# Kernel tuning notes

Measured on AMD Instinct MI355X. Metric: run time of the kernel, lower is better.

Reference implementation:

```python
import jax, jax.numpy as jnp
import numpy as np

B, C, N, K, G = 4, 128, 4096, 9, 4


def setup_inputs() -> dict:
    key = jax.random.key(0)
    ks = jax.random.split(key, 4)
    s = 0.05
    return {
        "features": jax.random.normal(ks[0], (B, C, N, 1), jnp.float32),
        # Attn.linear: Conv2d(2C -> C, 1x1)
        "w_lin": jax.random.normal(ks[1], (C, 2 * C), jnp.float32) * s,
        "b_lin": jnp.zeros((C,), jnp.float32),
        # atten_weight_conv: Linear(C -> K*G)
        "w_aw": jax.random.normal(ks[2], (K * G, C), jnp.float32) * s,
        "b_aw": jnp.zeros((K * G,), jnp.float32),
        # GroupNorm(4, C)
        "gn_g": jnp.ones((C,), jnp.float32),
        "gn_b": jnp.zeros((C,), jnp.float32),
        # conv: Conv2d(C -> C, 1x1) + BatchNorm2d(C)
        "conv_w": jax.random.normal(ks[3], (C, C), jnp.float32) * s,
        "conv_b": jnp.zeros((C,), jnp.float32),
        "bn_g": jnp.ones((C,), jnp.float32),
        "bn_b": jnp.zeros((C,), jnp.float32),
    }


def reference(features, w_lin, b_lin, w_aw, b_aw, gn_g, gn_b, conv_w, conv_b, bn_g, bn_b):
    B, C, N, _ = features.shape
    K, G = 9, 4
    Cg = C // G  # 32 channels per group
    EPS = 1e-5

    x = features[..., 0]                       # [B,C,N]
    # ---- KNN graph (negative squared distance, top-k) ----
    xx = jnp.sum(x * x, axis=1)                # [B,N]
    inner = jnp.einsum('bcn,bcm->bnm', x, x)   # [B,N,N]
    pd = 2.0 * inner - xx[:, :, None] - xx[:, None, :]
    idx = jax.lax.top_k(pd, K)[1]              # [B,N,K]

    # ---- edge feature gather: cat(x, x - x_neighbor) ----
    xt = x.transpose(0, 2, 1)                  # [B,N,C]
    b_ix = jnp.arange(B)[:, None, None]
    nbr = xt[b_ix, idx]                        # [B,N,K,C]
    ctr = jnp.broadcast_to(xt[:, :, None, :], (B, N, K, C))
    edge = jnp.concatenate([ctr, ctr - nbr], axis=-1)   # [B,N,K,2C]

    # ---- Attn.linear (1x1 conv == per-position linear) ----
    feat = jnp.einsum('bnke,ce->bnkc', edge, w_lin) + b_lin  # [B,N,K,C]

    # ---- grouped channel attention (4 groups of 32) ----
    fg = feat.reshape(B, N, K, G, Cg)
    scores = jnp.einsum('bnkgc,bnjgc->bngkj', fg, fg) / np.sqrt(32.0)
    s = jax.nn.softmax(scores, axis=-1)        # [B,N,G,K,K]
    attn = jnp.einsum('bngkj,bnjgc->bngkc', s, jax.nn.elu(fg))  # [B,N,G,K,Cg]

    # ---- attention weights over neighbors ----
    aw = jnp.einsum('bnc,dc->bnd', xt, w_aw) + b_aw          # [B,N,K*G]
    aw = jax.nn.softmax(aw.reshape(B, N, G, K), axis=-1)     # [B,N,G,K]

    # ---- weighted neighbor combine ----
    lf = jnp.einsum('bngk,bngkc->bngc', aw, attn)            # [B,N,G,Cg]
    lf = lf.transpose(0, 2, 3, 1).reshape(B, C, N, 1)        # [B,C,N,1]

    # ---- GroupNorm(4, C) over residual ----
    y = lf + features
    yg = y.reshape(B, G, Cg * N)
    mu = yg.mean(-1, keepdims=True)
    var = yg.var(-1, keepdims=True)
    yn = ((yg - mu) / jnp.sqrt(var + EPS)).reshape(B, C, N, 1)
    yn = yn * gn_g[None, :, None, None] + gn_b[None, :, None, None]

    # ---- 1x1 conv + BatchNorm (training-mode batch stats) + ReLU ----
    z = jnp.einsum('oc,bcnk->bonk', conv_w, yn) + conv_b[None, :, None, None]
    m = z.mean(axis=(0, 2, 3), keepdims=True)
    v = z.var(axis=(0, 2, 3), keepdims=True)
    z = (z - m) / jnp.sqrt(v + EPS) * bn_g[None, :, None, None] + bn_b[None, :, None, None]
    return jax.nn.relu(z)
```

## Files before the change

kernel.cpp:

```cpp
#include <hip/hip_runtime.h>
#include <hip/hip_bf16.h>
#include <cstddef>

#define NPTS 4096
#define CCH  128
#define KNN  9
#define GRP  4
#define BB   4
#define OFF_XT    0u
#define OFF_XX    2097152u
#define OFF_XHI   2113536u
#define OFF_IDX   3162112u
#define OFF_O     3309568u
#define OFF_Y     8159232u
#define OFF_GNP   10256384u
#define OFF_GNA   10387456u
#define OFF_GND   10387968u
#define OFF_WP    10388480u
#define OFF_BIASP 10454016u
#define OFF_BNSUM 10454528u
#define OFF_BNSQ  10454656u
#define OFF_BNSC  10454784u
#define OFF_BNSH  10454912u

using bf16x8 = __attribute__((ext_vector_type(8))) short;
using f32x4  = __attribute__((ext_vector_type(4))) float;

typedef __attribute__((address_space(1))) const unsigned as1c_u32;
typedef __attribute__((address_space(3))) unsigned as3_u32;

#define CE(a, b) { float _h = fmaxf(a, b); b = fminf(a, b); a = _h; }

#define SENT_BITS 0xFF7FF000u

__global__ void k_transpose(const float* __restrict__ x, float* __restrict__ xt,
                            __hip_bfloat16* __restrict__ xhi, float* __restrict__ xx) {
  __shared__ float t[32][33];
  int tx = threadIdx.x, ty = threadIdx.y;
  int n0 = blockIdx.x * 32, c0 = blockIdx.y * 32, b = blockIdx.z;
  float v = x[((size_t)b * CCH + c0 + ty) * NPTS + n0 + tx];
  t[ty][tx] = v;
  __syncthreads();
  float tv = t[tx][ty];
  size_t R = (size_t)b * NPTS + n0 + ty;
  int c = c0 + tx;
  xt[R * CCH + c] = tv;
  int g = c >> 3, w = c & 7;
  int sc = (((g ^ ((n0 + ty) & 15)) << 3) | w);
  xhi[R * CCH + sc] = __float2bfloat16(tv);
  if (ty == 0) {
    float s = 0.f;
    #pragma unroll
    for (int k = 0; k < 32; k++) { float u = t[k][tx]; s += u * u; }
    atomicAdd(&xx[b * NPTS + n0 + tx], s);
  }
}

__launch_bounds__(256, 2)
__global__ void k_knn(const short* __restrict__ xhi, const float* __restrict__ xx,
                      float* __restrict__ cand) {
  __shared__ short Acs[2][16384];
  const int tid = threadIdx.x;
  const int wave = tid >> 6, lane = tid & 63;
  const int quad = lane >> 4, m = lane & 15;
  const int b = blockIdx.y;
  const int q0 = blockIdx.x * 32;
  const short* xb = xhi + (size_t)b * NPTS * CCH;
  const float* xxb = xx + (b << 12);

  const char* gsrc0 = (const char*)xb + wave * 8192 + lane * 16;

  #pragma unroll
  for (int i = 0; i < 8; i++)
    __builtin_amdgcn_global_load_lds((as1c_u32*)(gsrc0 + i * 1024),
                                     (as3_u32*)&Acs[0][wave * 4096 + i * 512],
                                     16, 0, 0);

  bf16x8 qfrag[2][4];
  #pragma unroll
  for (int qt = 0; qt < 2; qt++) {
    const short* qrow = xb + (size_t)(q0 + qt * 16 + m) * CCH;
    #pragma unroll
    for (int ks = 0; ks < 4; ks++) {
      int slot = (ks * 4 + quad) ^ m;
      qfrag[qt][ks] = *(const bf16x8*)(qrow + slot * 8);
    }
  }

  float top8[2][8];
  #pragma unroll
  for (int qt = 0; qt < 2; qt++)
    #pragma unroll
    for (int p = 0; p < 8; p++) top8[qt][p] = __uint_as_float(SENT_BITS);

  for (int c = 0; c < 32; c++) {
    __syncthreads();
    if (c < 31) {
      const char* gsrc = gsrc0 + (size_t)(c + 1) * 32768;
      int bi = (c + 1) & 1;
      #pragma unroll
      for (int i = 0; i < 8; i++)
        __builtin_amdgcn_global_load_lds((as1c_u32*)(gsrc + i * 1024),
                                         (as3_u32*)&Acs[bi][wave * 4096 + i * 512],
                                         16, 0, 0);
    }
    f32x4 cinit[2];
    #pragma unroll
    for (int ct = 0; ct < 2; ct++)
      #pragma unroll
      for (int r = 0; r < 4; r++)
        cinit[ct][r] = -0.5f * xxb[c * 128 + wave * 32 + ct * 16 + quad * 4 + r];

    const short* cur = &Acs[c & 1][0];
    f32x4 acc[2][2];
    #pragma unroll
    for (int ct = 0; ct < 2; ct++)
      #pragma unroll
      for (int qt = 0; qt < 2; qt++) acc[ct][qt] = cinit[ct];

    #pragma unroll
    for (int ks = 0; ks < 4; ks++) {
      bf16x8 af[2];
      #pragma unroll
      for (int ct = 0; ct < 2; ct++) {
        int row = wave * 32 + ct * 16 + m;
        int slot = (ks * 4 + quad) ^ m;
        af[ct] = *(const bf16x8*)&cur[row * 128 + slot * 8];
      }
      #pragma unroll
      for (int ct = 0; ct < 2; ct++)
        #pragma unroll
        for (int qt = 0; qt < 2; qt++)
          acc[ct][qt] = __builtin_amdgcn_mfma_f32_16x16x32_bf16(
              af[ct], qfrag[qt][ks], acc[ct][qt], 0, 0, 0);
    }

    const unsigned cbase = (unsigned)(c * 128 + wave * 32 + quad * 4);
    #pragma unroll
    for (int qt = 0; qt < 2; qt++) {
      float k[8];
      #pragma unroll
      for (int ct = 0; ct < 2; ct++)
        #pragma unroll
        for (int r = 0; r < 4; r++) {
          unsigned u = __float_as_uint(acc[ct][qt][r]);
          k[ct * 4 + r] = __uint_as_float((u & 0xFFFFF000u) |
                                          (cbase + (unsigned)(ct * 16 + r)));
        }
      CE(k[0],k[1]) CE(k[2],k[3]) CE(k[4],k[5]) CE(k[6],k[7])
      CE(k[0],k[2]) CE(k[1],k[3]) CE(k[4],k[6]) CE(k[5],k[7])
      CE(k[1],k[2]) CE(k[5],k[6])
      CE(k[0],k[4]) CE(k[1],k[5]) CE(k[2],k[6]) CE(k[3],k[7])
      CE(k[2],k[4]) CE(k[3],k[5])
      CE(k[1],k[2]) CE(k[3],k[4]) CE(k[5],k[6])
      float t[8];
      #pragma unroll
      for (int i = 0; i < 8; i++) t[i] = fmaxf(top8[qt][i], k[7 - i]);
      CE(t[0],t[4]) CE(t[1],t[5]) CE(t[2],t[6]) CE(t[3],t[7])
      CE(t[0],t[2]) CE(t[1],t[3]) CE(t[4],t[6]) CE(t[5],t[7])
      CE(t[0],t[1]) CE(t[2],t[3]) CE(t[4],t[5]) CE(t[6],t[7])
      #pragma unroll
      for (int i = 0; i < 8; i++) top8[qt][i] = t[i];
    }
  }

  int slot = wave * 4 + quad;
  #pragma unroll
  for (int qt = 0; qt < 2; qt++) {
    int q = q0 + qt * 16 + m;
    float* dst = cand + ((size_t)((b << 12) + q) * 16 + slot) * 8;
    #pragma unroll
    for (int p = 0; p < 8; p++) dst[p] = top8[qt][p];
  }
}

__launch_bounds__(256)
__global__ void k_rerank(const float* __restrict__ cand, const float* __restrict__ xt,
                         const float* __restrict__ xx, int* __restrict__ idxOut) {
  __shared__ __align__(16) float arr[4][128];
  __shared__ int selS[4][16];
  __shared__ float keyS[4][16];
  int tid = threadIdx.x, wave = tid >> 6, lane = tid & 63;
  int qg = blockIdx.x * 4 + wave;
  int b = qg >> 12;
  const float* src = cand + (size_t)qg * 128;
  float e1 = src[lane], e2 = src[lane + 64];
  arr[wave][lane] = e1; arr[wave][lane + 64] = e2;
  __syncthreads();
  int r1 = 0, r2 = 0;
  #pragma unroll 8
  for (int f = 0; f < 128; f += 4) {
    float4 fv = *(const float4*)&arr[wave][f];
    r1 += (fv.x > e1) + (fv.y > e1) + (fv.z > e1) + (fv.w > e1);
    r2 += (fv.x > e2) + (fv.y > e2) + (fv.z > e2) + (fv.w > e2);
  }
  if (r1 < 16) selS[wave][r1] = (int)(__float_as_uint(e1) & 0xFFFu);
  if (r2 < 16) selS[wave][r2] = (int)(__float_as_uint(e2) & 0xFFFu);
  __syncthreads();
  int cnum = lane >> 2, part = lane & 3;
  int cidx = selS[wave][cnum];
  const float* rq = xt + (size_t)qg * CCH;
  const float* rc = xt + ((size_t)(b << 12) + cidx) * CCH;
  float dot = 0.f;
  #pragma unroll
  for (int j = 0; j < 8; j++) {
    float4 a4 = *(const float4*)&rq[part * 32 + j * 4];
    float4 c4 = *(const float4*)&rc[part * 32 + j * 4];
    dot += a4.x * c4.x + a4.y * c4.y + a4.z * c4.z + a4.w * c4.w;
  }
  dot += __shfl_xor(dot, 1);
  dot += __shfl_xor(dot, 2);
  if (part == 0)
    keyS[wave][cnum] = fmaf(2.f, dot, -xx[(b << 12) + cidx]);
  __syncthreads();
  if (lane < 16) {
    float k = keyS[wave][lane]; int i = selS[wave][lane];
    int r = 0;
    #pragma unroll
    for (int f = 0; f < 16; f++) {
      float fk = keyS[wave][f]; int fi = selS[wave][f];
      r += (fk > k) || (fk == k && fi < i);
    }
    if (r < 9) idxOut[(size_t)qg * 9 + r] = i;
  }
}

__launch_bounds__(256)
__global__ void k_linear(const float* __restrict__ xt, const float* __restrict__ w_lin,
                         const float* __restrict__ b_lin, const float* __restrict__ w_aw,
                         const float* __restrict__ b_aw, float* __restrict__ O) {
  __shared__ __align__(16) float Xs[64 * 132];
  __shared__ __align__(16) float Ws[64 * 132];
  int tid = threadIdx.x;
  int tx = tid & 15, ty = tid >> 4;
  int p0 = blockIdx.x * 64, o0 = blockIdx.y * 64;
  #pragma unroll
  for (int i = 0; i < 8; i++) {
    int flat = tid + i * 256; int r = flat >> 5, c4 = flat & 31;
    *(float4*)&Xs[r * 132 + c4 * 4] = *(const float4*)&xt[(size_t)(p0 + r) * CCH + c4 * 4];
  }
  #pragma unroll
  for (int i = 0; i < 8; i++) {
    int flat = tid + i * 256; int r = flat >> 5, c4 = flat & 31;
    int o = o0 + r; float4 v;
    if (o < 128) {
      float4 a = *(const float4*)&w_lin[(size_t)o * 256 + c4 * 4];
      float4 c = *(const float4*)&w_lin[(size_t)o * 256 + 128 + c4 * 4];
      v = make_float4(a.x + c.x, a.y + c.y, a.z + c.z, a.w + c.w);
    } else if (o < 256) {
      v = *(const float4*)&w_lin[(size_t)(o - 128) * 256 + 128 + c4 * 4];
    } else if (o < 292) {
      v = *(const float4*)&w_aw[(size_t)(o - 256) * 128 + c4 * 4];
    } else v = make_float4(0.f, 0.f, 0.f, 0.f);
    *(float4*)&Ws[r * 132 + c4 * 4] = v;
  }
  __syncthreads();
  float acc[4][4] = {};
  #pragma unroll 2
  for (int kq = 0; kq < 32; kq++) {
    float4 xa[4], wb[4];
    #pragma unroll
    for (int i = 0; i < 4; i++) xa[i] = *(const float4*)&Xs[(ty * 4 + i) * 132 + kq * 4];
    #pragma unroll
    for (int j = 0; j < 4; j++) wb[j] = *(const float4*)&Ws[(tx + 16 * j) * 132 + kq * 4];
    #pragma unroll
    for (int i = 0; i < 4; i++)
      #pragma unroll
      for (int j = 0; j < 4; j++)
        acc[i][j] += xa[i].x * wb[j].x + xa[i].y * wb[j].y + xa[i].z * wb[j].z + xa[i].w * wb[j].w;
  }
  #pragma unroll
  for (int j = 0; j < 4; j++) {
    int o = o0 + tx + 16 * j;
    if (o < 292) {
      float bias = (o < 128) ? b_lin[o] : ((o < 256) ? 0.f : b_aw[o - 256]);
      #pragma unroll
      for (int i = 0; i < 4; i++)
        O[(size_t)(p0 + ty * 4 + i) * 296 + o] = acc[i][j] + bias;
    }
  }
}

__launch_bounds__(256)
__global__ void k_attn(const float* __restrict__ O, const int* __restrict__ idxArr,
                       const float* __restrict__ xt, float* __restrict__ Y,
                       float* __restrict__ gnPart) {
  __shared__ __align__(16) float fF[4][1188];
  __shared__ __align__(16) float scS[4][432];
  __shared__ float awS[4][48];
  __shared__ float w9S[4][48];
  __shared__ int tI[45], tJ[45];
  int tid = threadIdx.x;
  int wave = tid >> 6, l = tid & 63;
  int pos = blockIdx.x * 4 + wave;
  int b = pos >> 12;
  if (tid == 0) {
    int p = 0;
    for (int i = 0; i < 9; i++) for (int j = i; j < 9; j++) { tI[p] = i; tJ[p] = j; p++; }
  }
  int nbr[9];
  const float* Op = O + (size_t)pos * 296;
  #pragma unroll
  for (int k = 0; k < 9; k++) nbr[k] = idxArr[(size_t)pos * 9 + k];
  float2 u = *(const float2*)(Op + 2 * l);
  float* fFw = fF[wave];
  #pragma unroll
  for (int k = 0; k < 9; k++) {
    const float* vp = O + (size_t)((b << 12) + nbr[k]) * 296 + 128;
    float2 vv = *(const float2*)(vp + 2 * l);
    *(float2*)&fFw[k * 132 + 2 * l] = make_float2(u.x - vv.x, u.y - vv.y);
  }
  __syncthreads();
  #pragma unroll
  for (int r = 0; r < 3; r++) {
    int p = r * 64 + l;
    if (p < 180) {
      int g = p / 45, q = p - g * 45;
      int i = tI[q], j = tJ[q];
      const float* fi = fFw + i * 132 + g * 32;
      const float* fj = fFw + j * 132 + g * 32;
      float s = 0.f;
      #pragma unroll
      for (int t8 = 0; t8 < 8; t8++) {
        float4 a4 = *(const float4*)(fi + 4 * t8);
        float4 b4 = *(const float4*)(fj + 4 * t8);
        s += a4.x * b4.x + a4.y * b4.y + a4.z * b4.z + a4.w * b4.w;
      }
      s *= 0.17677669529663687f;
      scS[wave][(g * 9 + i) * 12 + j] = s;
      scS[wave][(g * 9 + j) * 12 + i] = s;
    }
  }
  __syncthreads();
  if (l < 36) {
    int g = l / 9, i = l - g * 9;
    float* rp = &scS[wave][(g * 9 + i) * 12];
    float mx = rp[0];
    #pragma unroll
    for (int j = 1; j < 9; j++) mx = fmaxf(mx, rp[j]);
    float e[9]; float sm = 0.f;
    #pragma unroll
    for (int j = 0; j < 9; j++) { e[j] = __expf(rp[j] - mx); sm += e[j]; }
    float inv = 1.f / sm;
    #pragma unroll
    for (int j = 0; j < 9; j++) rp[j] = e[j] * inv;
  } else if (l < 40) {
    int g = l - 36;
    float a[9]; float mx = -3.4e38f;
    #pragma unroll
    for (int k = 0; k < 9; k++) { a[k] = Op[256 + g * 9 + k]; mx = fmaxf(mx, a[k]); }
    float sm = 0.f;
    #pragma unroll
    for (int k = 0; k < 9; k++) { a[k] = __expf(a[k] - mx); sm += a[k]; }
    float inv = 1.f / sm;
    #pragma unroll
    for (int k = 0; k < 9; k++) awS[wave][g * 12 + k] = a[k] * inv;
  }
  __syncthreads();
  if (l < 36) {
    int g = l / 9, j = l - g * 9;
    float s = 0.f;
    #pragma unroll
    for (int i = 0; i < 9; i++) s += awS[wave][g * 12 + i] * scS[wave][(g * 9 + i) * 12 + j];
    w9S[wave][g * 12 + j] = s;
  }
  __syncthreads();
  int g = l >> 4;
  float w9r[9];
  #pragma unroll
  for (int j = 0; j < 9; j++) w9r[j] = w9S[wave][g * 12 + j];
  int c0 = 2 * l;
  float lf0 = 0.f, lf1 = 0.f;
  #pragma unroll
  for (int j = 0; j < 9; j++) {
    float2 f2 = *(const float2*)&fFw[j * 132 + c0];
    float e0 = f2.x > 0.f ? f2.x : __expf(f2.x) - 1.f;
    float e1 = f2.y > 0.f ? f2.y : __expf(f2.y) - 1.f;
    lf0 += w9r[j] * e0;
    lf1 += w9r[j] * e1;
  }
  float2 xv = *(const float2*)(xt + (size_t)pos * CCH + c0);
  float y0 = lf0 + xv.x, y1 = lf1 + xv.y;
  *(float2*)(Y + (size_t)pos * CCH + c0) = make_float2(y0, y1);
  float s1 = y0 + y1, s2 = y0 * y0 + y1 * y1;
  #pragma unroll
  for (int mm = 1; mm <= 8; mm <<= 1) { s1 += __shfl_xor(s1, mm); s2 += __shfl_xor(s2, mm); }
  if ((l & 15) == 0) {
    gnPart[(size_t)pos * 8 + g * 2]     = s1;
    gnPart[(size_t)pos * 8 + g * 2 + 1] = s2;
  }
}

__global__ void k_gnstats(const float* __restrict__ gnPart,
                          const float* __restrict__ gn_g, const float* __restrict__ gn_b,
                          float* __restrict__ gnA, float* __restrict__ gnD) {
  int bg = blockIdx.x; int b = bg >> 2, g = bg & 3;
  int tid = threadIdx.x;
  float s1 = 0.f, s2 = 0.f;
  for (int r = tid; r < NPTS; r += 256) {
    const float* p = gnPart + (size_t)(b * NPTS + r) * 8 + g * 2;
    s1 += p[0]; s2 += p[1];
  }
  __shared__ float r1[256], r2[256];
  r1[tid] = s1; r2[tid] = s2;
  __syncthreads();
  for (int off = 128; off > 0; off >>= 1) {
    if (tid < off) { r1[tid] += r1[tid + off]; r2[tid] += r2[tid + off]; }
    __syncthreads();
  }
  __shared__ float muS, rsS;
  if (tid == 0) {
    float mu = r1[0] * (1.f / 131072.f);
    float var = r2[0] * (1.f / 131072.f) - mu * mu;
    muS = mu; rsS = 1.f / sqrtf(var + 1e-5f);
  }
  __syncthreads();
  if (tid < 32) {
    int c = g * 32 + tid;
    float a = rsS * gn_g[c];
    gnA[b * 128 + c] = a;
    gnD[b * 128 + c] = gn_b[c] - muS * a;
  }
}

__global__ void k_fold(const float* __restrict__ conv_w, const float* __restrict__ conv_b,
                       const float* __restrict__ gnA, const float* __restrict__ gnD,
                       float* __restrict__ Wp, float* __restrict__ biasp) {
  int b = blockIdx.x; int tid = threadIdx.x;
  __shared__ float dS[128], aS[128];
  if (tid < 128) { dS[tid] = gnD[b * 128 + tid]; aS[tid] = gnA[b * 128 + tid]; }
  __syncthreads();
  for (int f = tid; f < 16384; f += 256)
    Wp[(size_t)b * 16384 + f] = conv_w[f] * aS[f & 127];
  if (tid < 128) {
    float s = conv_b[tid];
    for (int c = 0; c < 128; c++) s += conv_w[tid * 128 + c] * dS[c];
    biasp[b * 128 + tid] = s;
  }
}

__launch_bounds__(256)
__global__ void k_conv(const float* __restrict__ Y, const float* __restrict__ Wp,
                       const float* __restrict__ biasp, float* __restrict__ zpre,
                       float* __restrict__ bnSum, float* __restrict__ bnSq) {
  __shared__ __align__(16) float Ys[64 * 132];
  __shared__ __align__(16) float Ws[64 * 132];
  int tid = threadIdx.x;
  int tx = tid & 15, ty = tid >> 4;
  int n0 = blockIdx.x * 64, o0 = blockIdx.y * 64, b = blockIdx.z;
  #pragma unroll
  for (int i = 0; i < 8; i++) {
    int flat = tid + i * 256; int r = flat >> 5, c4 = flat & 31;
    *(float4*)&Ys[r * 132 + c4 * 4] = *(const float4*)&Y[(size_t)((b << 12) + n0 + r) * CCH + c4 * 4];
    *(float4*)&Ws[r * 132 + c4 * 4] = *(const float4*)&Wp[(size_t)b * 16384 + (size_t)(o0 + r) * 128 + c4 * 4];
  }
  __syncthreads();
  float acc[4][4] = {};
  #pragma unroll 2
  for (int kq = 0; kq < 32; kq++) {
    float4 wa[4], yb[4];
    #pragma unroll
    for (int i = 0; i < 4; i++) wa[i] = *(const float4*)&Ws[(ty * 4 + i) * 132 + kq * 4];
    #pragma unroll
    for (int j = 0; j < 4; j++) yb[j] = *(const float4*)&Ys[(tx + 16 * j) * 132 + kq * 4];
    #pragma unroll
    for (int i = 0; i < 4; i++)
      #pragma unroll
      for (int j = 0; j < 4; j++)
        acc[i][j] += wa[i].x * yb[j].x + wa[i].y * yb[j].y + wa[i].z * yb[j].z + wa[i].w * yb[j].w;
  }
  #pragma unroll
  for (int i = 0; i < 4; i++) {
    int o = o0 + ty * 4 + i;
    float bias = biasp[b * 128 + o];
    float p1 = 0.f, p2 = 0.f;
    #pragma unroll
    for (int j = 0; j < 4; j++) {
      float z = acc[i][j] + bias;
      zpre[(((size_t)((b << 7) + o)) << 12) + n0 + tx + 16 * j] = z;
      p1 += z; p2 += z * z;
    }
    #pragma unroll
    for (int mm = 1; mm <= 8; mm <<= 1) { p1 += __shfl_xor(p1, mm); p2 += __shfl_xor(p2, mm); }
    if (tx == 0) { atomicAdd(&bnSum[o], p1); atomicAdd(&bnSq[o], p2); }
  }
}

__global__ void k_bnfin(const float* __restrict__ bnSum, const float* __restrict__ bnSq,
                        const float* __restrict__ bn_g, const float* __restrict__ bn_b,
                        float* __restrict__ bnScale, float* __restrict__ bnShift) {
  int o = threadIdx.x;
  float m = bnSum[o] * (1.f / 16384.f);
  float v = bnSq[o] * (1.f / 16384.f) - m * m;
  float sc = bn_g[o] / sqrtf(v + 1e-5f);
  bnScale[o] = sc;
  bnShift[o] = bn_b[o] - m * sc;
}

__global__ void k_final(const float* __restrict__ zpre, const float* __restrict__ bnScale,
                        const float* __restrict__ bnShift, float* __restrict__ out) {
  int i4 = blockIdx.x * 256 + threadIdx.x;
  int e = i4 * 4;
  int o = (e >> 12) & 127;
  float4 z = *(const float4*)&zpre[e];
  float sc = bnScale[o], sh = bnShift[o];
  float4 r;
  r.x = fmaxf(fmaf(z.x, sc, sh), 0.f);
  r.y = fmaxf(fmaf(z.y, sc, sh), 0.f);
  r.z = fmaxf(fmaf(z.z, sc, sh), 0.f);
  r.w = fmaxf(fmaf(z.w, sc, sh), 0.f);
  *(float4*)&out[e] = r;
}

extern "C" void kernel_launch(void* const* d_in, const int* in_sizes, int n_in,
                              void* d_out, int out_size, void* d_ws, size_t ws_size,
                              hipStream_t stream) {
  const float* features = (const float*)d_in[0];
  const float* w_lin  = (const float*)d_in[1];
  const float* b_lin  = (const float*)d_in[2];
  const float* w_aw   = (const float*)d_in[3];
  const float* b_aw   = (const float*)d_in[4];
  const float* gn_g   = (const float*)d_in[5];
  const float* gn_b   = (const float*)d_in[6];
  const float* conv_w = (const float*)d_in[7];
  const float* conv_b = (const float*)d_in[8];
  const float* bn_g   = (const float*)d_in[9];
  const float* bn_b   = (const float*)d_in[10];

  float* ws    = (float*)d_ws;
  float* xt    = ws + OFF_XT;
  float* xxp   = ws + OFF_XX;
  __hip_bfloat16* xhip = (__hip_bfloat16*)(ws + OFF_XHI);
  int*   idxp  = (int*)(ws + OFF_IDX);
  float* Op    = ws + OFF_O;
  float* candp = ws + OFF_O;
  float* Yp    = ws + OFF_Y;
  float* gnp   = ws + OFF_GNP;
  float* gnA   = ws + OFF_GNA;
  float* gnD   = ws + OFF_GND;
  float* Wp    = ws + OFF_WP;
  float* biasp = ws + OFF_BIASP;
  float* bnSum = ws + OFF_BNSUM;
  float* bnSq  = ws + OFF_BNSQ;
  float* bnSc  = ws + OFF_BNSC;
  float* bnSh  = ws + OFF_BNSH;
  float* zpre  = xt;

  hipMemsetAsync(xxp, 0, NPTS * BB * sizeof(float), stream);
  hipMemsetAsync(bnSum, 0, 256 * sizeof(float), stream);

  k_transpose<<<dim3(128, 4, 4), dim3(32, 32), 0, stream>>>(features, xt, xhip, xxp);
  k_knn<<<dim3(128, 4), 256, 0, stream>>>((const short*)xhip, xxp, candp);
  k_rerank<<<4096, 256, 0, stream>>>(candp, xt, xxp, idxp);
  k_linear<<<dim3(256, 5), 256, 0, stream>>>(xt, w_lin, b_lin, w_aw, b_aw, Op);
  k_attn<<<4096, 256, 0, stream>>>(Op, idxp, xt, Yp, gnp);
  k_gnstats<<<16, 256, 0, stream>>>(gnp, gn_g, gn_b, gnA, gnD);
  k_fold<<<4, 256, 0, stream>>>(conv_w, conv_b, gnA, gnD, Wp, biasp);
  k_conv<<<dim3(64, 2, 4), 256, 0, stream>>>(Yp, Wp, biasp, zpre, bnSum, bnSq);
  k_bnfin<<<1, 128, 0, stream>>>(bnSum, bnSq, bn_g, bn_b, bnSc, bnSh);
  k_final<<<2048, 256, 0, stream>>>(zpre, bnSc, bnSh, (float*)d_out);
}
```

Measured before the change: 276.8 us.

## Load KNN tiles directly to registers and fuse small stats kernels

The KNN kernel drops its LDS double buffer filled by global_load_lds plus block barriers. Each wave now loads its candidate fragments straight from global memory into registers, ping-ponging two register buffers. Separately, the GroupNorm stats kernel is merged into the weight-fold kernel, and the BatchNorm finalize is folded into the final elementwise kernel, removing two launches. The trade-offs are more registers and uncoalesced direct global loads in the KNN loop, and every thread of the final kernel recomputing the BN scale.

After: 281.1 us. About the same (+1.6%).

```diff
diff --git a/kernel.cpp b/kernel.cpp
--- a/kernel.cpp
+++ b/kernel.cpp
@@ -14,20 +14,13 @@
 #define OFF_O     3309568u
 #define OFF_Y     8159232u
 #define OFF_GNP   10256384u
-#define OFF_GNA   10387456u
-#define OFF_GND   10387968u
 #define OFF_WP    10388480u
 #define OFF_BIASP 10454016u
 #define OFF_BNSUM 10454528u
 #define OFF_BNSQ  10454656u
-#define OFF_BNSC  10454784u
-#define OFF_BNSH  10454912u
 
 using bf16x8 = __attribute__((ext_vector_type(8))) short;
 using f32x4  = __attribute__((ext_vector_type(4))) float;
-
-typedef __attribute__((address_space(1))) const unsigned as1c_u32;
-typedef __attribute__((address_space(3))) unsigned as3_u32;
 
 #define CE(a, b) { float _h = fmaxf(a, b); b = fminf(a, b); a = _h; }
 
@@ -56,10 +49,63 @@
   }
 }
 
+static __device__ __forceinline__ void knn_chunk(
+    int c, const uint4* __restrict__ buf, const float* __restrict__ xxb,
+    int wave, int quad, const bf16x8 (*qfrag)[4], float (*top8)[8]) {
+  f32x4 cinit[2];
+  #pragma unroll
+  for (int ct = 0; ct < 2; ct++)
+    #pragma unroll
+    for (int r = 0; r < 4; r++)
+      cinit[ct][r] = -0.5f * xxb[c * 128 + wave * 32 + ct * 16 + quad * 4 + r];
+  f32x4 acc[2][2];
+  #pragma unroll
+  for (int ct = 0; ct < 2; ct++)
+    #pragma unroll
+    for (int qt = 0; qt < 2; qt++) acc[ct][qt] = cinit[ct];
+  #pragma unroll
+  for (int ks = 0; ks < 4; ks++) {
+    #pragma unroll
+    for (int ct = 0; ct < 2; ct++) {
+      bf16x8 af = __builtin_bit_cast(bf16x8, buf[ct * 4 + ks]);
+      #pragma unroll
+      for (int qt = 0; qt < 2; qt++)
+        acc[ct][qt] = __builtin_amdgcn_mfma_f32_16x16x32_bf16(
+            af, qfrag[qt][ks], acc[ct][qt], 0, 0, 0);
+    }
+  }
+  const unsigned cbase = (unsigned)(c * 128 + wave * 32 + quad * 4);
+  #pragma unroll
+  for (int qt = 0; qt < 2; qt++) {
+    float k[8];
+    #pragma unroll
+    for (int ct = 0; ct < 2; ct++)
+      #pragma unroll
+      for (int r = 0; r < 4; r++) {
+        unsigned u = __float_as_uint(acc[ct][qt][r]);
+        k[ct * 4 + r] = __uint_as_float((u & 0xFFFFF000u) |
+                                        (cbase + (unsigned)(ct * 16 + r)));
+      }
+    CE(k[0],k[1]) CE(k[2],k[3]) CE(k[4],k[5]) CE(k[6],k[7])
+    CE(k[0],k[2]) CE(k[1],k[3]) CE(k[4],k[6]) CE(k[5],k[7])
+    CE(k[1],k[2]) CE(k[5],k[6])
+    CE(k[0],k[4]) CE(k[1],k[5]) CE(k[2],k[6]) CE(k[3],k[7])
+    CE(k[2],k[4]) CE(k[3],k[5])
+    CE(k[1],k[2]) CE(k[3],k[4]) CE(k[5],k[6])
+    float t[8];
+    #pragma unroll
+    for (int i = 0; i < 8; i++) t[i] = fmaxf(top8[qt][i], k[7 - i]);
+    CE(t[0],t[4]) CE(t[1],t[5]) CE(t[2],t[6]) CE(t[3],t[7])
+    CE(t[0],t[2]) CE(t[1],t[3]) CE(t[4],t[6]) CE(t[5],t[7])
+    CE(t[0],t[1]) CE(t[2],t[3]) CE(t[4],t[5]) CE(t[6],t[7])
+    #pragma unroll
+    for (int i = 0; i < 8; i++) top8[qt][i] = t[i];
+  }
+}
+
 __launch_bounds__(256, 2)
 __global__ void k_knn(const short* __restrict__ xhi, const float* __restrict__ xx,
                       float* __restrict__ cand) {
-  __shared__ short Acs[2][16384];
   const int tid = threadIdx.x;
   const int wave = tid >> 6, lane = tid & 63;
   const int quad = lane >> 4, m = lane & 15;
@@ -68,14 +114,6 @@
   const short* xb = xhi + (size_t)b * NPTS * CCH;
   const float* xxb = xx + (b << 12);
 
-  const char* gsrc0 = (const char*)xb + wave * 8192 + lane * 16;
-
-  #pragma unroll
-  for (int i = 0; i < 8; i++)
-    __builtin_amdgcn_global_load_lds((as1c_u32*)(gsrc0 + i * 1024),
-                                     (as3_u32*)&Acs[0][wave * 4096 + i * 512],
-                                     16, 0, 0);
-
   bf16x8 qfrag[2][4];
   #pragma unroll
   for (int qt = 0; qt < 2; qt++) {
@@ -93,76 +131,29 @@
     #pragma unroll
     for (int p = 0; p < 8; p++) top8[qt][p] = __uint_as_float(SENT_BITS);
 
-  for (int c = 0; c < 32; c++) {
-    __syncthreads();
-    if (c < 31) {
-      const char* gsrc = gsrc0 + (size_t)(c + 1) * 32768;
-      int bi = (c + 1) & 1;
-      #pragma unroll
-      for (int i = 0; i < 8; i++)
-        __builtin_amdgcn_global_load_lds((as1c_u32*)(gsrc + i * 1024),
-                                         (as3_u32*)&Acs[bi][wave * 4096 + i * 512],
-                                         16, 0, 0);
-    }
-    f32x4 cinit[2];
-    #pragma unroll
-    for (int ct = 0; ct < 2; ct++)
-      #pragma unroll
-      for (int r = 0; r < 4; r++)
-        cinit[ct][r] = -0.5f * xxb[c * 128 + wave * 32 + ct * 16 + quad * 4 + r];
-
-    const short* cur = &Acs[c & 1][0];
-    f32x4 acc[2][2];
-    #pragma unroll
-    for (int ct = 0; ct < 2; ct++)
-      #pragma unroll
-      for (int qt = 0; qt < 2; qt++) acc[ct][qt] = cinit[ct];
-
-    #pragma unroll
-    for (int ks = 0; ks < 4; ks++) {
-      bf16x8 af[2];
-      #pragma unroll
-      for (int ct = 0; ct < 2; ct++) {
-        int row = wave * 32 + ct * 16 + m;
-        int slot = (ks * 4 + quad) ^ m;
-        af[ct] = *(const bf16x8*)&cur[row * 128 + slot * 8];
-      }
-      #pragma unroll
-      for (int ct = 0; ct < 2; ct++)
-        #pragma unroll
-        for (int qt = 0; qt < 2; qt++)
-          acc[ct][qt] = __builtin_amdgcn_mfma_f32_16x16x32_bf16(
-              af[ct], qfrag[qt][ks], acc[ct][qt], 0, 0, 0);
-    }
-
-    const unsigned cbase = (unsigned)(c * 128 + wave * 32 + quad * 4);
-    #pragma unroll
-    for (int qt = 0; qt < 2; qt++) {
-      float k[8];
-      #pragma unroll
-      for (int ct = 0; ct < 2; ct++)
-        #pragma unroll
-        for (int r = 0; r < 4; r++) {
-          unsigned u = __float_as_uint(acc[ct][qt][r]);
-          k[ct * 4 + r] = __uint_as_float((u & 0xFFFFF000u) |
-                                          (cbase + (unsigned)(ct * 16 + r)));
-        }
-      CE(k[0],k[1]) CE(k[2],k[3]) CE(k[4],k[5]) CE(k[6],k[7])
-      CE(k[0],k[2]) CE(k[1],k[3]) CE(k[4],k[6]) CE(k[5],k[7])
-      CE(k[1],k[2]) CE(k[5],k[6])
-      CE(k[0],k[4]) CE(k[1],k[5]) CE(k[2],k[6]) CE(k[3],k[7])
-      CE(k[2],k[4]) CE(k[3],k[5])
-      CE(k[1],k[2]) CE(k[3],k[4]) CE(k[5],k[6])
-      float t[8];
-      #pragma unroll
-      for (int i = 0; i < 8; i++) t[i] = fmaxf(top8[qt][i], k[7 - i]);
-      CE(t[0],t[4]) CE(t[1],t[5]) CE(t[2],t[6]) CE(t[3],t[7])
-      CE(t[0],t[2]) CE(t[1],t[3]) CE(t[4],t[6]) CE(t[5],t[7])
-      CE(t[0],t[1]) CE(t[2],t[3]) CE(t[4],t[5]) CE(t[6],t[7])
-      #pragma unroll
-      for (int i = 0; i < 8; i++) top8[qt][i] = t[i];
-    }
-  }
+  const short* abase = xb + (size_t)(wave * 32 + m) * CCH;
+  int goff[8];
+  #pragma unroll
+  for (int ct = 0; ct < 2; ct++)
+    #pragma unroll
+    for (int ks = 0; ks < 4; ks++)
+      goff[ct * 4 + ks] = ct * 16 * CCH + (((ks * 4 + quad) ^ m) * 8);
+
+#define KNN_LOAD(buf, cc) { \
+    const short* _p = abase + (size_t)(cc) * (128 * CCH); \
+    _Pragma("unroll") \
+    for (int _i = 0; _i < 8; _i++) (buf)[_i] = *(const uint4*)(_p + goff[_i]); }
+
+  uint4 bufA[8], bufB[8];
+  KNN_LOAD(bufA, 0)
+  #pragma unroll 1
+  for (int t = 0; t < 16; t++) {
+    KNN_LOAD(bufB, 2 * t + 1)
+    knn_chunk(2 * t, bufA, xxb, wave, quad, qfrag, top8);
+    if (t < 15) KNN_LOAD(bufA, 2 * t + 2)
+    knn_chunk(2 * t + 1, bufB, xxb, wave, quad, qfrag, top8);
+  }
+#undef KNN_LOAD
 
   int slot = wave * 4 + quad;
   #pragma unroll
@@ -391,44 +382,32 @@
   }
 }
 
-__global__ void k_gnstats(const float* __restrict__ gnPart,
-                          const float* __restrict__ gn_g, const float* __restrict__ gn_b,
-                          float* __restrict__ gnA, float* __restrict__ gnD) {
-  int bg = blockIdx.x; int b = bg >> 2, g = bg & 3;
-  int tid = threadIdx.x;
-  float s1 = 0.f, s2 = 0.f;
-  for (int r = tid; r < NPTS; r += 256) {
-    const float* p = gnPart + (size_t)(b * NPTS + r) * 8 + g * 2;
-    s1 += p[0]; s2 += p[1];
-  }
-  __shared__ float r1[256], r2[256];
-  r1[tid] = s1; r2[tid] = s2;
-  __syncthreads();
-  for (int off = 128; off > 0; off >>= 1) {
-    if (tid < off) { r1[tid] += r1[tid + off]; r2[tid] += r2[tid + off]; }
-    __syncthreads();
-  }
-  __shared__ float muS, rsS;
-  if (tid == 0) {
-    float mu = r1[0] * (1.f / 131072.f);
-    float var = r2[0] * (1.f / 131072.f) - mu * mu;
-    muS = mu; rsS = 1.f / sqrtf(var + 1e-5f);
-  }
-  __syncthreads();
-  if (tid < 32) {
-    int c = g * 32 + tid;
-    float a = rsS * gn_g[c];
-    gnA[b * 128 + c] = a;
-    gnD[b * 128 + c] = gn_b[c] - muS * a;
-  }
-}
-
-__global__ void k_fold(const float* __restrict__ conv_w, const float* __restrict__ conv_b,
-                       const float* __restrict__ gnA, const float* __restrict__ gnD,
-                       float* __restrict__ Wp, float* __restrict__ biasp) {
+__global__ void k_gnfold(const float* __restrict__ gnPart,
+                         const float* __restrict__ gn_g, const float* __restrict__ gn_b,
+                         const float* __restrict__ conv_w, const float* __restrict__ conv_b,
+                         float* __restrict__ Wp, float* __restrict__ biasp) {
   int b = blockIdx.x; int tid = threadIdx.x;
-  __shared__ float dS[128], aS[128];
-  if (tid < 128) { dS[tid] = gnD[b * 128 + tid]; aS[tid] = gnA[b * 128 + tid]; }
+  int wave = tid >> 6, lane = tid & 63;
+  __shared__ float aS[128], dS[128];
+  {
+    int g = wave;
+    float s1 = 0.f, s2 = 0.f;
+    for (int r = lane; r < NPTS; r += 64) {
+      float2 p = *(const float2*)&gnPart[(size_t)(b * NPTS + r) * 8 + g * 2];
+      s1 += p.x; s2 += p.y;
+    }
+    #pragma unroll
+    for (int off = 1; off < 64; off <<= 1) { s1 += __shfl_xor(s1, off); s2 += __shfl_xor(s2, off); }
+    float mu = s1 * (1.f / 131072.f);
+    float var = s2 * (1.f / 131072.f) - mu * mu;
+    float rs = 1.f / sqrtf(var + 1e-5f);
+    if (lane < 32) {
+      int c = g * 32 + lane;
+      float a = rs * gn_g[c];
+      aS[c] = a;
+      dS[c] = gn_b[c] - mu * a;
+    }
+  }
   __syncthreads();
   for (int f = tid; f < 16384; f += 256)
     Wp[(size_t)b * 16384 + f] = conv_w[f] * aS[f & 127];
@@ -486,24 +465,17 @@
   }
 }
 
-__global__ void k_bnfin(const float* __restrict__ bnSum, const float* __restrict__ bnSq,
-                        const float* __restrict__ bn_g, const float* __restrict__ bn_b,
-                        float* __restrict__ bnScale, float* __restrict__ bnShift) {
-  int o = threadIdx.x;
+__global__ void k_final(const float* __restrict__ zpre, const float* __restrict__ bnSum,
+                        const float* __restrict__ bnSq, const float* __restrict__ bn_g,
+                        const float* __restrict__ bn_b, float* __restrict__ out) {
+  int i4 = blockIdx.x * 256 + threadIdx.x;
+  int e = i4 * 4;
+  int o = (e >> 12) & 127;
   float m = bnSum[o] * (1.f / 16384.f);
   float v = bnSq[o] * (1.f / 16384.f) - m * m;
   float sc = bn_g[o] / sqrtf(v + 1e-5f);
-  bnScale[o] = sc;
-  bnShift[o] = bn_b[o] - m * sc;
-}
-
-__global__ void k_final(const float* __restrict__ zpre, const float* __restrict__ bnScale,
-                        const float* __restrict__ bnShift, float* __restrict__ out) {
-  int i4 = blockIdx.x * 256 + threadIdx.x;
-  int e = i4 * 4;
-  int o = (e >> 12) & 127;
+  float sh = bn_b[o] - m * sc;
   float4 z = *(const float4*)&zpre[e];
-  float sc = bnScale[o], sh = bnShift[o];
   float4 r;
   r.x = fmaxf(fmaf(z.x, sc, sh), 0.f);
   r.y = fmaxf(fmaf(z.y, sc, sh), 0.f);
@@ -536,14 +508,10 @@
   float* candp = ws + OFF_O;
   float* Yp    = ws + OFF_Y;
   float* gnp   = ws + OFF_GNP;
-  float* gnA   = ws + OFF_GNA;
-  float* gnD   = ws + OFF_GND;
   float* Wp    = ws + OFF_WP;
   float* biasp = ws + OFF_BIASP;
   float* bnSum = ws + OFF_BNSUM;
   float* bnSq  = ws + OFF_BNSQ;
-  float* bnSc  = ws + OFF_BNSC;
-  float* bnSh  = ws + OFF_BNSH;
   float* zpre  = xt;
 
   hipMemsetAsync(xxp, 0, NPTS * BB * sizeof(float), stream);
@@ -554,9 +522,7 @@
   k_rerank<<<4096, 256, 0, stream>>>(candp, xt, xxp, idxp);
   k_linear<<<dim3(256, 5), 256, 0, stream>>>(xt, w_lin, b_lin, w_aw, b_aw, Op);
   k_attn<<<4096, 256, 0, stream>>>(Op, idxp, xt, Yp, gnp);
-  k_gnstats<<<16, 256, 0, stream>>>(gnp, gn_g, gn_b, gnA, gnD);
-  k_fold<<<4, 256, 0, stream>>>(conv_w, conv_b, gnA, gnD, Wp, biasp);
+  k_gnfold<<<4, 256, 0, stream>>>(gnp, gn_g, gn_b, conv_w, conv_b, Wp, biasp);
   k_conv<<<dim3(64, 2, 4), 256, 0, stream>>>(Yp, Wp, biasp, zpre, bnSum, bnSq);
-  k_bnfin<<<1, 128, 0, stream>>>(bnSum, bnSq, bn_g, bn_b, bnSc, bnSh);
-  k_final<<<2048, 256, 0, stream>>>(zpre, bnSc, bnSh, (float*)d_out);
-}
+  k_final<<<2048, 256, 0, stream>>>(zpre, bnSum, bnSq, bn_g, bn_b, (float*)d_out);
+}
```
